# Performance work log

Hardware: AMD Instinct MI355X
Metric: run time of the kernel (lower is better)

Reference implementation:

```python
import jax, jax.numpy as jnp
import numpy as np

H, W_BINS = 8, 8
EPS = 1e-6
EXTREMA = ((-1.0, 1.0), (-1.0, 1.0))


def setup_inputs() -> dict:
    key = jax.random.key(0)
    k1, k2, k3 = jax.random.split(key, 3)
    B, N, C = 4, 65536, 256
    values = jax.random.normal(k1, (B, N, C), dtype=jnp.float32)
    # coords sampled inside the fixed extrema so the bucketization is in-range
    coords = jax.random.uniform(k2, (N, 2), dtype=jnp.float32, minval=-1.0, maxval=1.0)
    W = jax.random.normal(k3, (H * W_BINS * C, 512), dtype=jnp.float32) * 0.01
    b = jnp.zeros((512,), dtype=jnp.float32)
    return {"values": values, "coords": coords, "W": W, "b": b}


def reference(values, coords, W, b):
    B, N, C = values.shape
    hw = H * W_BINS
    # bin edges, matching torch.linspace(extrema-eps, extrema+eps, steps=h+1)
    Tx = jnp.linspace(EXTREMA[0][0] - EPS, EXTREMA[0][1] + EPS, H + 1)
    Ty = jnp.linspace(EXTREMA[1][0] - EPS, EXTREMA[1][1] + EPS, W_BINS + 1)
    # kx = index of first edge strictly greater than x  (== (Tx <= X).min(-1) argmin)
    kx = jnp.searchsorted(Tx, coords[:, 0], side="right")
    ky = jnp.searchsorted(Ty, coords[:, 1], side="right")
    bins = (kx - 1) + (ky - 1) * H  # [N], in [0, hw)

    # fused segment-mean over all bins in one pass (replaces the per-bin loop)
    vals_nf = values.transpose(1, 0, 2).reshape(N, B * C)  # [N, B*C]
    sums = jax.ops.segment_sum(vals_nf, bins, num_segments=hw)  # [hw, B*C]
    counts = jax.ops.segment_sum(jnp.ones((N,), values.dtype), bins, num_segments=hw)
    means = sums / jnp.maximum(counts, 1.0)[:, None]  # [hw, B*C]
    # cat([ [B,C] for b in range(hw) ], dim=1) -> [B, hw*C]
    out = means.reshape(hw, B, C).transpose(1, 0, 2).reshape(B, hw * C)
    return out @ W + b
```

## Files before the change

### kernel.cpp

```cpp
#include <hip/hip_runtime.h>
#include <cstddef>

#define NPTS   65536
#define BATCH  4
#define CH     256
#define HWBINS 64
#define KDIM   16384
#define JDIM   512
#define CHUNK  64
#define SSLOTS 8
#define GSLOTS 64
#define ZERO_F4 ((SSLOTS * BATCH * KDIM + GSLOTS * 2048) / 4)

typedef float vf4 __attribute__((ext_vector_type(4)));
typedef float vf2 __attribute__((ext_vector_type(2)));

__device__ __forceinline__ float4 ntload4(const float* p) {
    vf4 v = __builtin_nontemporal_load((const vf4*)p);
    return make_float4(v.x, v.y, v.z, v.w);
}
__device__ __forceinline__ float2 ntload2(const float* p) {
    vf2 v = __builtin_nontemporal_load((const vf2*)p);
    return make_float2(v.x, v.y);
}

__device__ __forceinline__ int bucket1d(float xf) {
    const double start = -1.0 - 1e-6;
    const double stop  =  1.0 + 1e-6;
    const double step  = (stop - start) / 8.0;
    double x = (double)xf;
    int k = 0;
#pragma unroll
    for (int i = 0; i < 8; ++i) k += ((double)i * step + start <= x) ? 1 : 0;
    k += (stop <= x) ? 1 : 0;
    int b = k - 1;
    return b < 0 ? 0 : (b > 7 ? 7 : b);
}

__global__ __launch_bounds__(256) void k_bins(const float* __restrict__ coords,
                                              int* __restrict__ bins,
                                              int* __restrict__ hist_blk,
                                              float4* __restrict__ zero4) {
    __shared__ int s_h[HWBINS];
    const int tid = threadIdx.x;
    const int blk = blockIdx.x;
    {
        const float4 z = make_float4(0.f, 0.f, 0.f, 0.f);
        for (int i = blk * 256 + tid; i < ZERO_F4; i += 64 * 256)
            zero4[i] = z;
    }
    if (tid < HWBINS) s_h[tid] = 0;
    __syncthreads();
#pragma unroll
    for (int i = 0; i < 4; ++i) {
        int n = blk * 1024 + i * 256 + tid;
        float2 xy = *(const float2*)(coords + 2 * (size_t)n);
        int bx = bucket1d(xy.x);
        int by = bucket1d(xy.y);
        int bin = by * 8 + bx;
        bins[n] = bin;
        atomicAdd(&s_h[bin], 1);
    }
    __syncthreads();
    if (tid < HWBINS) hist_blk[blk * HWBINS + tid] = s_h[tid];
}

__global__ void k_scan(const int* __restrict__ hist_blk,
                       int* __restrict__ counts,
                       int* __restrict__ block_base) {
    const int b = threadIdx.x;
    int tot = 0;
#pragma unroll 8
    for (int blk = 0; blk < 64; ++blk) tot += hist_blk[blk * HWBINS + b];
    counts[b] = tot;
    int inc = tot;
#pragma unroll
    for (int d = 1; d < 64; d <<= 1) {
        int v = __shfl_up(inc, d, 64);
        if (b >= d) inc += v;
    }
    int run = inc - tot;
#pragma unroll 8
    for (int blk = 0; blk < 64; ++blk) {
        int h = hist_blk[blk * HWBINS + b];
        block_base[blk * HWBINS + b] = run;
        run += h;
    }
}

__global__ __launch_bounds__(256) void k_scatter(const int* __restrict__ bins,
                                                 const int* __restrict__ block_base,
                                                 int2* __restrict__ pairs) {
    __shared__ int s_cur[HWBINS];
    const int tid = threadIdx.x;
    const int blk = blockIdx.x;
    if (tid < HWBINS) s_cur[tid] = block_base[blk * HWBINS + tid];
    __syncthreads();
#pragma unroll
    for (int i = 0; i < 4; ++i) {
        int n = blk * 1024 + i * 256 + tid;
        int bin = bins[n];
        int pos = atomicAdd(&s_cur[bin], 1);
        pairs[pos] = make_int2(n, bin);
    }
}

__global__ __launch_bounds__(256) void k_seg(const float* __restrict__ values,
                                             const int2* __restrict__ pairs,
                                             float* __restrict__ sums8) {
    __shared__ int2 sp[CHUNK];
    const int tid = threadIdx.x;
    const int r0  = blockIdx.x * CHUNK;
    if (tid < CHUNK) sp[tid] = pairs[r0 + tid];
    __syncthreads();

    const int w    = tid >> 6;
    const int lane = tid & 63;
    const int slot = blockIdx.x & (SSLOTS - 1);
    const float* vb = values + (size_t)w * NPTS * CH + lane * 4;
    float* sb = sums8 + (size_t)slot * BATCH * KDIM + (size_t)w * KDIM + lane * 4;

    float4 acc = make_float4(0.f, 0.f, 0.f, 0.f);
    int cur = sp[0].y;

    auto flushfn = [&](int nb) {
        float* d = sb + (size_t)cur * CH;
        unsafeAtomicAdd(d + 0, acc.x);
        unsafeAtomicAdd(d + 1, acc.y);
        unsafeAtomicAdd(d + 2, acc.z);
        unsafeAtomicAdd(d + 3, acc.w);
        acc = make_float4(0.f, 0.f, 0.f, 0.f);
        cur = nb;
    };

    float4 a[8], nx[8];
#pragma unroll
    for (int j = 0; j < 8; ++j)
        a[j] = ntload4(vb + (size_t)sp[j].x * CH);

#pragma unroll
    for (int g = 0; g < CHUNK; g += 8) {
        if (g + 8 < CHUNK) {
#pragma unroll
            for (int j = 0; j < 8; ++j)
                nx[j] = ntload4(vb + (size_t)sp[g + 8 + j].x * CH);
        }
#pragma unroll
        for (int j = 0; j < 8; ++j) {
            int bj = sp[g + j].y;
            if (bj != cur) flushfn(bj);
            acc.x += a[j].x; acc.y += a[j].y; acc.z += a[j].z; acc.w += a[j].w;
        }
        if (g + 8 < CHUNK) {
#pragma unroll
            for (int j = 0; j < 8; ++j) a[j] = nx[j];
        }
    }
    flushfn(cur);
}

__global__ __launch_bounds__(256) void k_gemm_a(const float* __restrict__ Wm,
                                                const float* __restrict__ sums8,
                                                const int* __restrict__ counts,
                                                float* __restrict__ out_part) {
    __shared__ float s_m[4 * 32];
    const int tid = threadIdx.x;
    const int kc  = blockIdx.x;
    const int k0  = kc * 32;
    if (tid < 128) {
        int bb = tid >> 5, kk = tid & 31, k = k0 + kk;
        float s = 0.f;
#pragma unroll
        for (int sl = 0; sl < SSLOTS; ++sl)
            s += sums8[(size_t)sl * BATCH * KDIM + (size_t)bb * KDIM + k];
        float cnt = (float)counts[k >> 8];
        s_m[tid] = s / fmaxf(cnt, 1.0f);
    }
    __syncthreads();

    const float* wp = Wm + (size_t)k0 * JDIM + 2 * tid;
    float2 a0 = {0.f, 0.f}, a1 = {0.f, 0.f}, a2 = {0.f, 0.f}, a3 = {0.f, 0.f};
#pragma unroll
    for (int kk = 0; kk < 32; ++kk) {
        float2 w = ntload2(wp + (size_t)kk * JDIM);
        float m0 = s_m[kk], m1 = s_m[32 + kk], m2 = s_m[64 + kk], m3 = s_m[96 + kk];
        a0.x += m0 * w.x; a0.y += m0 * w.y;
        a1.x += m1 * w.x; a1.y += m1 * w.y;
        a2.x += m2 * w.x; a2.y += m2 * w.y;
        a3.x += m3 * w.x; a3.y += m3 * w.y;
    }
    const int slot = kc & (GSLOTS - 1);
    float* op = out_part + (size_t)slot * 2048 + 2 * tid;
    unsafeAtomicAdd(op + 0,    a0.x); unsafeAtomicAdd(op + 1,    a0.y);
    unsafeAtomicAdd(op + 512,  a1.x); unsafeAtomicAdd(op + 513,  a1.y);
    unsafeAtomicAdd(op + 1024, a2.x); unsafeAtomicAdd(op + 1025, a2.y);
    unsafeAtomicAdd(op + 1536, a3.x); unsafeAtomicAdd(op + 1537, a3.y);
}

__global__ __launch_bounds__(256) void k_gemm_b(const float* __restrict__ out_part,
                                                const float* __restrict__ bias,
                                                float* __restrict__ out) {
    const int idx = blockIdx.x * 256 + threadIdx.x;
    const int j = idx & 511;
    float s = bias[j];
#pragma unroll
    for (int sl = 0; sl < GSLOTS; ++sl) s += out_part[(size_t)sl * 2048 + idx];
    out[idx] = s;
}

extern "C" void kernel_launch(void* const* d_in, const int* in_sizes, int n_in,
                              void* d_out, int out_size, void* d_ws, size_t ws_size,
                              hipStream_t stream) {
    const float* values = (const float*)d_in[0];
    const float* coords = (const float*)d_in[1];
    const float* Wm     = (const float*)d_in[2];
    const float* bias   = (const float*)d_in[3];
    float* out = (float*)d_out;

    char* ws = (char*)d_ws;
    int*   bins       = (int*)(ws + 0);
    int*   hist_blk   = (int*)(ws + 262144);
    int*   counts     = (int*)(ws + 278528);
    int*   block_base = (int*)(ws + 278784);
    int2*  pairs      = (int2*)(ws + 295168);
    float* sums8      = (float*)(ws + 819456);
    float* out_part   = (float*)(ws + 2916608);

    k_bins   <<<64, 256, 0, stream>>>(coords, bins, hist_blk, (float4*)sums8);
    k_scan   <<<1, 64, 0, stream>>>(hist_blk, counts, block_base);
    k_scatter<<<64, 256, 0, stream>>>(bins, block_base, pairs);
    k_seg    <<<NPTS / CHUNK, 256, 0, stream>>>(values, pairs, sums8);
    k_gemm_a <<<512, 256, 0, stream>>>(Wm, sums8, counts, out_part);
    k_gemm_b <<<8, 256, 0, stream>>>(out_part, bias, out);
}
```

Measured before the change: 393.5 us.

## Replace sort-and-gather segment sum with streaming LDS-atomic per-block partials

Drops the scan/scatter counting sort and the gathered row reads. Each block now streams a contiguous chunk of rows for one batch and accumulates every bin in a 64 KB shared-memory array through LDS atomics, then writes a full partial sum for the reduction in the GEMM stage. This turns scattered row gathers into coalesced streaming reads and removes two kernels, at the cost of per-element LDS atomic contention, lower occupancy from the large shared buffer, and 256 partial arrays that gemm_a must sum.

```diff
diff --git a/kernel.cpp b/kernel.cpp
--- a/kernel.cpp
+++ b/kernel.cpp
@@ -7,18 +7,18 @@
 #define HWBINS 64
 #define KDIM   16384
 #define JDIM   512
-#define CHUNK  64
-#define SSLOTS 8
 #define GSLOTS 64
-#define ZERO_F4 ((SSLOTS * BATCH * KDIM + GSLOTS * 2048) / 4)
+
+#define SEGGRID 256
+#define SEGTHR  512
+#define CHUNKS_PER_B   (SEGGRID / BATCH)
+#define ROWS_PER_CHUNK (NPTS / CHUNKS_PER_B)
+#define ROWS_PER_WAVE  (ROWS_PER_CHUNK / (SEGTHR/64))
+#define ZERO_F4 (GSLOTS * 2048 / 4)
 
 typedef float vf4 __attribute__((ext_vector_type(4)));
 typedef float vf2 __attribute__((ext_vector_type(2)));
 
-__device__ __forceinline__ float4 ntload4(const float* p) {
-    vf4 v = __builtin_nontemporal_load((const vf4*)p);
-    return make_float4(v.x, v.y, v.z, v.w);
-}
 __device__ __forceinline__ float2 ntload2(const float* p) {
     vf2 v = __builtin_nontemporal_load((const vf2*)p);
     return make_float2(v.x, v.y);
@@ -65,102 +65,81 @@
     if (tid < HWBINS) hist_blk[blk * HWBINS + tid] = s_h[tid];
 }
 
-__global__ void k_scan(const int* __restrict__ hist_blk,
-                       int* __restrict__ counts,
-                       int* __restrict__ block_base) {
+__global__ void k_counts(const int* __restrict__ hist_blk,
+                         int* __restrict__ counts) {
     const int b = threadIdx.x;
     int tot = 0;
 #pragma unroll 8
     for (int blk = 0; blk < 64; ++blk) tot += hist_blk[blk * HWBINS + b];
     counts[b] = tot;
-    int inc = tot;
-#pragma unroll
-    for (int d = 1; d < 64; d <<= 1) {
-        int v = __shfl_up(inc, d, 64);
-        if (b >= d) inc += v;
-    }
-    int run = inc - tot;
-#pragma unroll 8
-    for (int blk = 0; blk < 64; ++blk) {
-        int h = hist_blk[blk * HWBINS + b];
-        block_base[blk * HWBINS + b] = run;
-        run += h;
-    }
-}
-
-__global__ __launch_bounds__(256) void k_scatter(const int* __restrict__ bins,
-                                                 const int* __restrict__ block_base,
-                                                 int2* __restrict__ pairs) {
-    __shared__ int s_cur[HWBINS];
-    const int tid = threadIdx.x;
-    const int blk = blockIdx.x;
-    if (tid < HWBINS) s_cur[tid] = block_base[blk * HWBINS + tid];
-    __syncthreads();
-#pragma unroll
-    for (int i = 0; i < 4; ++i) {
-        int n = blk * 1024 + i * 256 + tid;
-        int bin = bins[n];
-        int pos = atomicAdd(&s_cur[bin], 1);
-        pairs[pos] = make_int2(n, bin);
-    }
-}
-
-__global__ __launch_bounds__(256) void k_seg(const float* __restrict__ values,
-                                             const int2* __restrict__ pairs,
-                                             float* __restrict__ sums8) {
-    __shared__ int2 sp[CHUNK];
-    const int tid = threadIdx.x;
-    const int r0  = blockIdx.x * CHUNK;
-    if (tid < CHUNK) sp[tid] = pairs[r0 + tid];
-    __syncthreads();
-
-    const int w    = tid >> 6;
+}
+
+__global__ __launch_bounds__(SEGTHR) void k_seg(const float* __restrict__ values,
+                                                const int* __restrict__ bins,
+                                                float* __restrict__ partials) {
+    __shared__ float s_acc[KDIM];
+    const int tid   = threadIdx.x;
+    const int b     = blockIdx.x >> 6;
+    const int chunk = blockIdx.x & 63;
+    const int r0    = chunk * ROWS_PER_CHUNK;
+    {
+        float4* s4 = (float4*)s_acc;
+        const float4 z = make_float4(0.f, 0.f, 0.f, 0.f);
+#pragma unroll
+        for (int i = tid; i < KDIM / 4; i += SEGTHR) s4[i] = z;
+    }
+    __syncthreads();
+
+    const int wid  = tid >> 6;
     const int lane = tid & 63;
-    const int slot = blockIdx.x & (SSLOTS - 1);
-    const float* vb = values + (size_t)w * NPTS * CH + lane * 4;
-    float* sb = sums8 + (size_t)slot * BATCH * KDIM + (size_t)w * KDIM + lane * 4;
-
-    float4 acc = make_float4(0.f, 0.f, 0.f, 0.f);
-    int cur = sp[0].y;
-
-    auto flushfn = [&](int nb) {
-        float* d = sb + (size_t)cur * CH;
-        unsafeAtomicAdd(d + 0, acc.x);
-        unsafeAtomicAdd(d + 1, acc.y);
-        unsafeAtomicAdd(d + 2, acc.z);
-        unsafeAtomicAdd(d + 3, acc.w);
-        acc = make_float4(0.f, 0.f, 0.f, 0.f);
-        cur = nb;
-    };
-
-    float4 a[8], nx[8];
-#pragma unroll
-    for (int j = 0; j < 8; ++j)
-        a[j] = ntload4(vb + (size_t)sp[j].x * CH);
-
-#pragma unroll
-    for (int g = 0; g < CHUNK; g += 8) {
-        if (g + 8 < CHUNK) {
-#pragma unroll
-            for (int j = 0; j < 8; ++j)
-                nx[j] = ntload4(vb + (size_t)sp[g + 8 + j].x * CH);
+    const int wr0  = r0 + wid * ROWS_PER_WAVE;
+    const float* vb = values + ((size_t)b * NPTS + wr0) * CH + lane * 2;
+    const int*   bp = bins + wr0;
+
+    float2 aA[8], aB[8], nA[8], nB[8];
+    int ab[8], nb[8];
+#pragma unroll
+    for (int j = 0; j < 8; ++j) {
+        aA[j] = ntload2(vb + (size_t)j * CH);
+        aB[j] = ntload2(vb + (size_t)j * CH + 128);
+        ab[j] = bp[j];
+    }
+#pragma unroll
+    for (int g = 0; g < ROWS_PER_WAVE; g += 8) {
+        if (g + 8 < ROWS_PER_WAVE) {
+#pragma unroll
+            for (int j = 0; j < 8; ++j) {
+                nA[j] = ntload2(vb + (size_t)(g + 8 + j) * CH);
+                nB[j] = ntload2(vb + (size_t)(g + 8 + j) * CH + 128);
+                nb[j] = bp[g + 8 + j];
+            }
         }
 #pragma unroll
         for (int j = 0; j < 8; ++j) {
-            int bj = sp[g + j].y;
-            if (bj != cur) flushfn(bj);
-            acc.x += a[j].x; acc.y += a[j].y; acc.z += a[j].z; acc.w += a[j].w;
+            float* d = s_acc + ab[j] * CH + lane * 2;
+            atomicAdd(d + 0,   aA[j].x);
+            atomicAdd(d + 1,   aA[j].y);
+            atomicAdd(d + 128, aB[j].x);
+            atomicAdd(d + 129, aB[j].y);
         }
-        if (g + 8 < CHUNK) {
-#pragma unroll
-            for (int j = 0; j < 8; ++j) a[j] = nx[j];
+        if (g + 8 < ROWS_PER_WAVE) {
+#pragma unroll
+            for (int j = 0; j < 8; ++j) {
+                aA[j] = nA[j]; aB[j] = nB[j]; ab[j] = nb[j];
+            }
         }
     }
-    flushfn(cur);
+    __syncthreads();
+    {
+        const float4* s4 = (const float4*)s_acc;
+        float4* p4 = (float4*)(partials + (size_t)blockIdx.x * KDIM);
+#pragma unroll
+        for (int i = tid; i < KDIM / 4; i += SEGTHR) p4[i] = s4[i];
+    }
 }
 
 __global__ __launch_bounds__(256) void k_gemm_a(const float* __restrict__ Wm,
-                                                const float* __restrict__ sums8,
+                                                const float* __restrict__ partials,
                                                 const int* __restrict__ counts,
                                                 float* __restrict__ out_part) {
     __shared__ float s_m[4 * 32];
@@ -170,9 +149,9 @@
     if (tid < 128) {
         int bb = tid >> 5, kk = tid & 31, k = k0 + kk;
         float s = 0.f;
-#pragma unroll
-        for (int sl = 0; sl < SSLOTS; ++sl)
-            s += sums8[(size_t)sl * BATCH * KDIM + (size_t)bb * KDIM + k];
+#pragma unroll 8
+        for (int c = 0; c < CHUNKS_PER_B; ++c)
+            s += partials[(size_t)(bb * CHUNKS_PER_B + c) * KDIM + k];
         float cnt = (float)counts[k >> 8];
         s_m[tid] = s / fmaxf(cnt, 1.0f);
     }
@@ -218,18 +197,15 @@
     float* out = (float*)d_out;
 
     char* ws = (char*)d_ws;
-    int*   bins       = (int*)(ws + 0);
-    int*   hist_blk   = (int*)(ws + 262144);
-    int*   counts     = (int*)(ws + 278528);
-    int*   block_base = (int*)(ws + 278784);
-    int2*  pairs      = (int2*)(ws + 295168);
-    float* sums8      = (float*)(ws + 819456);
-    float* out_part   = (float*)(ws + 2916608);
-
-    k_bins   <<<64, 256, 0, stream>>>(coords, bins, hist_blk, (float4*)sums8);
-    k_scan   <<<1, 64, 0, stream>>>(hist_blk, counts, block_base);
-    k_scatter<<<64, 256, 0, stream>>>(bins, block_base, pairs);
-    k_seg    <<<NPTS / CHUNK, 256, 0, stream>>>(values, pairs, sums8);
-    k_gemm_a <<<512, 256, 0, stream>>>(Wm, sums8, counts, out_part);
-    k_gemm_b <<<8, 256, 0, stream>>>(out_part, bias, out);
-}
+    int*   bins     = (int*)(ws + 0);
+    int*   hist_blk = (int*)(ws + 262144);
+    int*   counts   = (int*)(ws + 278528);
+    float* out_part = (float*)(ws + 278784);
+    float* partials = (float*)(ws + 803072);
+
+    k_bins  <<<64, 256, 0, stream>>>(coords, bins, hist_blk, (float4*)out_part);
+    k_counts<<<1, 64, 0, stream>>>(hist_blk, counts);
+    k_seg   <<<SEGGRID, SEGTHR, 0, stream>>>(values, bins, partials);
+    k_gemm_a<<<512, 256, 0, stream>>>(Wm, partials, counts, out_part);
+    k_gemm_b<<<8, 256, 0, stream>>>(out_part, bias, out);
+}
```

New measurement: 678.9 us. 72.5% more time.
